# Performance work log

Hardware: AMD Instinct MI355X
Metric: run time of the kernel (lower is better)

## Reference

```python
import jax, jax.numpy as jnp
import numpy as np

B, T, C, H, W = 1, 8, 64, 256, 256
HD = 4            # heads; channels per head c = C // HD
PS = 7            # patch size (from wpsum config)
Q = 32768         # number of queries
K_TOT = 15        # neighbors provided
K = 10            # self.k -> slice to top-10
CH = C // HD


def setup_inputs() -> dict:
    key = jax.random.key(0)
    k1, k2, k3, k4, k5 = jax.random.split(key, 5)
    vid = jax.random.normal(k1, (B, T, C, H, W), jnp.float32)
    dists = jax.random.uniform(k2, (B, HD, Q, K_TOT), jnp.float32)
    t = jax.random.randint(k3, (B, HD, Q, K_TOT, 1), 0, T)
    hi = jax.random.randint(k4, (B, HD, Q, K_TOT, 1), 0, H - PS + 1)
    wi = jax.random.randint(k5, (B, HD, Q, K_TOT, 1), 0, W - PS + 1)
    inds = jnp.concatenate([t, hi, wi], axis=-1).astype(jnp.int32)
    return {"vid": vid, "dists": dists, "inds": inds}


def _gather_patches_head(vid_h, idx):
    # vid_h: [T, c, H, W]; idx: [Q, 3] -> patch [Q, c, ps, ps]
    t, hi, wi = idx[:, 0], idx[:, 1], idx[:, 2]
    pr = jnp.arange(PS)
    rows = hi[:, None, None] + pr[None, :, None]   # [Q, ps, 1]
    cols = wi[:, None, None] + pr[None, None, :]   # [Q, 1, ps]
    # advanced indexing split by ':' puts broadcast dims first -> [Q, ps, ps, c]
    patch = vid_h[t[:, None, None], :, rows, cols]
    return patch.transpose(0, 3, 1, 2)             # [Q, c, ps, ps]


_gather = jax.vmap(jax.vmap(_gather_patches_head))  # over B, HD


def reference(vid, dists, inds):
    # slice top-k neighbors (self.k > 0 path)
    dists = dists[..., :K]
    inds = inds[..., :K, :]
    # split channels across heads: [B, HD, T, c, H, W]
    vidh = vid.reshape(B, T, HD, CH, H, W).transpose(0, 2, 1, 3, 4, 5)
    d_k = jnp.moveaxis(dists, -1, 0)    # [K, B, HD, Q]
    i_k = jnp.moveaxis(inds, -2, 0)     # [K, B, HD, Q, 3]

    def step(acc, xk):
        w, idx = xk                      # w [B,HD,Q], idx [B,HD,Q,3]
        p = _gather(vidh, idx)           # [B, HD, Q, c, ps, ps]
        return acc + w[..., None, None, None] * p, None

    init = jnp.zeros((B, HD, Q, CH, PS, PS), vid.dtype)
    patches, _ = jax.lax.scan(step, init, (d_k, i_k))
    # rearrange 'b h q c ph pw -> (b q ph pw) (h c)'
    out = patches.transpose(0, 2, 4, 5, 1, 3).reshape(B * Q * PS * PS, HD * CH)
    return out
```

## Files before the change

kernel.cpp:

```cpp
#include <hip/hip_runtime.h>
#include <hip/hip_fp16.h>

#define T_    8
#define C_    64
#define H_    256
#define W_    256
#define HD_   4
#define CH_   16
#define PS_   7
#define Q_    32768
#define KTOT_ 15
#define K_    10
#define HW_   (H_*W_)

__global__ __launch_bounds__(256) void transcvt_kernel(
    const float* __restrict__ vid, __half* __restrict__ vidP) {
  __shared__ float tile[64][65];
  const int b  = blockIdx.x;
  const int wt = b & 3;
  const int h  = (b >> 2) & (H_ - 1);
  const int t  = b >> 10;
  const int w0 = wt * 64;

  const float* src = vid + (size_t)t * C_ * HW_ + (size_t)h * W_ + w0;
  const int wq = (threadIdx.x & 15) * 4;
  const int c0 = threadIdx.x >> 4;
  #pragma unroll
  for (int i = 0; i < 4; ++i) {
    const int c = c0 + i * 16;
    const float4 v = *reinterpret_cast<const float4*>(src + (size_t)c * HW_ + wq);
    tile[c][wq + 0] = v.x; tile[c][wq + 1] = v.y;
    tile[c][wq + 2] = v.z; tile[c][wq + 3] = v.w;
  }
  __syncthreads();

  const int cq = (threadIdx.x & 3) * 4;
  const int w  = threadIdx.x >> 2;
  #pragma unroll
  for (int hd = 0; hd < HD_; ++hd) {
    ushort4 pk;
    pk.x = __half_as_ushort(__float2half_rn(tile[hd * CH_ + cq + 0][w]));
    pk.y = __half_as_ushort(__float2half_rn(tile[hd * CH_ + cq + 1][w]));
    pk.z = __half_as_ushort(__float2half_rn(tile[hd * CH_ + cq + 2][w]));
    pk.w = __half_as_ushort(__float2half_rn(tile[hd * CH_ + cq + 3][w]));
    __half* dst = vidP +
        ((((size_t)hd * T_ + t) * H_ + h) * W_ + w0 + w) * CH_ + cq;
    *reinterpret_cast<ushort4*>(dst) = pk;
  }
}

__global__ __launch_bounds__(448) void wpsum_h_kernel(
    const __half* __restrict__ vsrc,
    const float* __restrict__ dists,
    const int*   __restrict__ inds,
    float*       __restrict__ out) {
  const int q   = blockIdx.x;
  const int tid = threadIdx.x;

  __shared__ int   s_off[HD_][K_];
  __shared__ float s_w[HD_][K_];
  if (tid < HD_ * K_) {
    const int hd = tid / K_, k = tid % K_;
    const int* ip = inds + (((size_t)hd * Q_ + q) * KTOT_ + k) * 3;
    s_off[hd][k] = ((((hd * T_ + ip[0]) * H_ + ip[1]) * W_) + ip[2]) * CH_;
    s_w[hd][k]   = dists[((size_t)hd * Q_ + q) * KTOT_ + k];
  }
  __syncthreads();

  const int lane = tid & 63;
  const int pi   = tid >> 6;
  const bool act = lane < 56;
  const int hd   = act ? (lane / 14) : 0;
  const int rem  = lane - hd * 14;
  const int psub = act ? (rem >> 1) : 0;
  const int hv   = rem & 1;
  const int lconst = (pi * W_ + psub) * CH_ + hv * 8;

  float wk[K_]; int off[K_];
  #pragma unroll
  for (int k = 0; k < K_; ++k) {
    wk[k]  = s_w[hd][k];
    off[k] = s_off[hd][k] + lconst;
  }

  float4 a[K_];
  if (act) {
    #pragma unroll
    for (int k = 0; k < K_; ++k)
      a[k] = *reinterpret_cast<const float4*>(vsrc + (size_t)off[k]);
  } else {
    #pragma unroll
    for (int k = 0; k < K_; ++k)
      a[k] = make_float4(0.f, 0.f, 0.f, 0.f);
  }

  float acc[8] = {0.f, 0.f, 0.f, 0.f, 0.f, 0.f, 0.f, 0.f};
  #pragma unroll
  for (int k = 0; k < K_; ++k) {
    const __half2* hp = reinterpret_cast<const __half2*>(&a[k]);
    #pragma unroll
    for (int j = 0; j < 4; ++j) {
      const float2 f = __half22float2(hp[j]);
      acc[2 * j + 0] = fmaf(wk[k], f.x, acc[2 * j + 0]);
      acc[2 * j + 1] = fmaf(wk[k], f.y, acc[2 * j + 1]);
    }
  }

  if (act) {
    float* ob = out + ((size_t)q * (PS_ * PS_) + pi * PS_ + psub) * (HD_ * CH_)
                    + hd * CH_ + hv * 8;
    *reinterpret_cast<float4*>(ob + 0) = make_float4(acc[0], acc[1], acc[2], acc[3]);
    *reinterpret_cast<float4*>(ob + 4) = make_float4(acc[4], acc[5], acc[6], acc[7]);
  }
}

__global__ __launch_bounds__(448) void wpsum_fallback_kernel(
    const float* __restrict__ vid,
    const float* __restrict__ dists,
    const int*   __restrict__ inds,
    float*       __restrict__ out) {
  const int q   = blockIdx.x;
  const int tid = threadIdx.x;

  __shared__ int   s_off[HD_][K_];
  __shared__ float s_w[HD_][K_];
  if (tid < HD_ * K_) {
    const int hd = tid / K_, k = tid % K_;
    const int* ip = inds + (((size_t)hd * Q_ + q) * KTOT_ + k) * 3;
    s_off[hd][k] = ((ip[0] * C_ + hd * CH_) * H_ + ip[1]) * W_ + ip[2];
    s_w[hd][k]   = dists[((size_t)hd * Q_ + q) * KTOT_ + k];
  }
  __syncthreads();

  const int lane = tid & 63;
  const int pi   = tid >> 6;
  const int hd   = lane >> 4;
  const int c    = lane & 15;

  float wk[K_]; int off[K_];
  #pragma unroll
  for (int k = 0; k < K_; ++k) {
    wk[k]  = s_w[hd][k];
    off[k] = s_off[hd][k] + c * HW_;
  }
  #pragma unroll
  for (int pj = 0; pj < PS_; ++pj) {
    const int d = pi * W_ + pj;
    float acc = 0.f;
    #pragma unroll
    for (int k = 0; k < K_; ++k)
      acc = fmaf(wk[k], vid[(size_t)(off[k] + d)], acc);
    out[((size_t)q * (PS_ * PS_) + pi * PS_ + pj) * (HD_ * CH_) + lane] = acc;
  }
}

extern "C" void kernel_launch(void* const* d_in, const int* in_sizes, int n_in,
                              void* d_out, int out_size, void* d_ws, size_t ws_size,
                              hipStream_t stream) {
  const float* vid   = (const float*)d_in[0];
  const float* dists = (const float*)d_in[1];
  const int*   inds  = (const int*)d_in[2];
  float*       out   = (float*)d_out;

  const size_t need = (size_t)HD_ * T_ * HW_ * CH_ * sizeof(__half);
  if (ws_size >= need) {
    __half* vidP = (__half*)d_ws;
    transcvt_kernel<<<T_ * H_ * (W_ / 64), 256, 0, stream>>>(vid, vidP);
    wpsum_h_kernel<<<Q_, 448, 0, stream>>>(vidP, dists, inds, out);
  } else {
    wpsum_fallback_kernel<<<Q_, 448, 0, stream>>>(vid, dists, inds, out);
  }
}
```

Measured before the change: 490.8 us.

## Sort neighbors by frame/row, stream gathers in pairs, use nontemporal output stores

Each head's 10 neighbors are now rank-sorted in shared memory by (t, row) key, so gathers from nearby rows are issued close together for better cache locality. The gather loop is restructured from ten loads issued at once to five non-unrolled iterations of two loads each, which lowers register pressure but gives up memory-level parallelism. Output writes switch to nontemporal stores so the large output stream does not pollute cache. The extra sort step adds a sync and some shared-memory work per block.

```diff
diff --git a/kernel.cpp b/kernel.cpp
--- a/kernel.cpp
+++ b/kernel.cpp
@@ -12,6 +12,8 @@
 #define KTOT_ 15
 #define K_    10
 #define HW_   (H_*W_)
+
+typedef float f32x4 __attribute__((ext_vector_type(4)));
 
 __global__ __launch_bounds__(256) void transcvt_kernel(
     const float* __restrict__ vid, __half* __restrict__ vidP) {
@@ -57,13 +59,32 @@
   const int q   = blockIdx.x;
   const int tid = threadIdx.x;
 
+  __shared__ int   s_key[HD_][K_];
+  __shared__ int   s_toff[HD_][K_];
+  __shared__ float s_tw[HD_][K_];
   __shared__ int   s_off[HD_][K_];
   __shared__ float s_w[HD_][K_];
+
   if (tid < HD_ * K_) {
     const int hd = tid / K_, k = tid % K_;
     const int* ip = inds + (((size_t)hd * Q_ + q) * KTOT_ + k) * 3;
-    s_off[hd][k] = ((((hd * T_ + ip[0]) * H_ + ip[1]) * W_) + ip[2]) * CH_;
-    s_w[hd][k]   = dists[((size_t)hd * Q_ + q) * KTOT_ + k];
+    const int t = ip[0], hi = ip[1], wi = ip[2];
+    s_key[hd][k]  = (t << 8) | hi;
+    s_toff[hd][k] = (((hd * T_ + t) * H_ + hi) * W_ + wi) * CH_;
+    s_tw[hd][k]   = dists[((size_t)hd * Q_ + q) * KTOT_ + k];
+  }
+  __syncthreads();
+  if (tid < HD_ * K_) {
+    const int hd = tid / K_, k = tid % K_;
+    const int key = s_key[hd][k];
+    int r = 0;
+    #pragma unroll
+    for (int j = 0; j < K_; ++j) {
+      const int kj = s_key[hd][j];
+      r += (kj < key) || (kj == key && j < k);
+    }
+    s_off[hd][r] = s_toff[hd][k];
+    s_w[hd][r]   = s_tw[hd][k];
   }
   __syncthreads();
 
@@ -72,45 +93,43 @@
   const bool act = lane < 56;
   const int hd   = act ? (lane / 14) : 0;
   const int rem  = lane - hd * 14;
-  const int psub = act ? (rem >> 1) : 0;
+  const int psub = rem >> 1;
   const int hv   = rem & 1;
   const int lconst = (pi * W_ + psub) * CH_ + hv * 8;
 
-  float wk[K_]; int off[K_];
-  #pragma unroll
-  for (int k = 0; k < K_; ++k) {
-    wk[k]  = s_w[hd][k];
-    off[k] = s_off[hd][k] + lconst;
-  }
+  float acc[8] = {0.f, 0.f, 0.f, 0.f, 0.f, 0.f, 0.f, 0.f};
 
-  float4 a[K_];
-  if (act) {
-    #pragma unroll
-    for (int k = 0; k < K_; ++k)
-      a[k] = *reinterpret_cast<const float4*>(vsrc + (size_t)off[k]);
-  } else {
-    #pragma unroll
-    for (int k = 0; k < K_; ++k)
-      a[k] = make_float4(0.f, 0.f, 0.f, 0.f);
-  }
-
-  float acc[8] = {0.f, 0.f, 0.f, 0.f, 0.f, 0.f, 0.f, 0.f};
-  #pragma unroll
-  for (int k = 0; k < K_; ++k) {
-    const __half2* hp = reinterpret_cast<const __half2*>(&a[k]);
+  #pragma unroll 1
+  for (int c = 0; c < K_ / 2; ++c) {
+    const float w0 = s_w[hd][2 * c + 0];
+    const float w1 = s_w[hd][2 * c + 1];
+    f32x4 a0 = {0.f, 0.f, 0.f, 0.f}, a1 = {0.f, 0.f, 0.f, 0.f};
+    if (act) {
+      a0 = *reinterpret_cast<const f32x4*>(
+          vsrc + (size_t)(s_off[hd][2 * c + 0] + lconst));
+      a1 = *reinterpret_cast<const f32x4*>(
+          vsrc + (size_t)(s_off[hd][2 * c + 1] + lconst));
+    }
+    const __half2* h0 = reinterpret_cast<const __half2*>(&a0);
+    const __half2* h1 = reinterpret_cast<const __half2*>(&a1);
     #pragma unroll
     for (int j = 0; j < 4; ++j) {
-      const float2 f = __half22float2(hp[j]);
-      acc[2 * j + 0] = fmaf(wk[k], f.x, acc[2 * j + 0]);
-      acc[2 * j + 1] = fmaf(wk[k], f.y, acc[2 * j + 1]);
+      const float2 f0 = __half22float2(h0[j]);
+      const float2 f1 = __half22float2(h1[j]);
+      acc[2 * j + 0] = fmaf(w0, f0.x, acc[2 * j + 0]);
+      acc[2 * j + 1] = fmaf(w0, f0.y, acc[2 * j + 1]);
+      acc[2 * j + 0] = fmaf(w1, f1.x, acc[2 * j + 0]);
+      acc[2 * j + 1] = fmaf(w1, f1.y, acc[2 * j + 1]);
     }
   }
 
   if (act) {
     float* ob = out + ((size_t)q * (PS_ * PS_) + pi * PS_ + psub) * (HD_ * CH_)
                     + hd * CH_ + hv * 8;
-    *reinterpret_cast<float4*>(ob + 0) = make_float4(acc[0], acc[1], acc[2], acc[3]);
-    *reinterpret_cast<float4*>(ob + 4) = make_float4(acc[4], acc[5], acc[6], acc[7]);
+    f32x4 v0 = {acc[0], acc[1], acc[2], acc[3]};
+    f32x4 v1 = {acc[4], acc[5], acc[6], acc[7]};
+    __builtin_nontemporal_store(v0, reinterpret_cast<f32x4*>(ob));
+    __builtin_nontemporal_store(v1, reinterpret_cast<f32x4*>(ob + 4));
   }
 }
 
```

Result: no change. 489.6 us (-0.2%).
